# Optimization experiments

Hardware: AMD Instinct MI355X
Metric: run time of the kernel (lower is better)

The kernel has to match this reference:

```python
import jax, jax.numpy as jnp
import numpy as np

N, S, D, K = 4, 2048, 512, 16  # batch, seq_len, d_model, d_state


def setup_inputs() -> dict:
    key = jax.random.key(0)
    ks = jax.random.split(key, 6)
    tokens = jax.random.normal(ks[0], (N, S, D), dtype=jnp.float32)
    log_A = jax.random.normal(ks[1], (D, K), dtype=jnp.float32) * 0.1
    W_B = jax.random.normal(ks[2], (K, D), dtype=jnp.float32) * (1.0 / np.sqrt(D))
    W_C = jax.random.normal(ks[3], (K, D), dtype=jnp.float32) * (1.0 / np.sqrt(D))
    W_delta = jax.random.normal(ks[4], (D, D), dtype=jnp.float32) * (1.0 / np.sqrt(D))
    b_delta = jax.random.normal(ks[5], (D,), dtype=jnp.float32) * 0.01
    return {"tokens": tokens, "log_A": log_A, "W_B": W_B, "W_C": W_C,
            "W_delta": W_delta, "b_delta": b_delta}


def _selective_scan(toks, log_A, W_B, W_C, W_delta, b_delta):
    # toks: [N,S,D]
    deltas = jax.nn.softplus(toks @ W_delta.T + b_delta)          # [N,S,D]
    Bs = toks @ W_B.T                                             # [N,S,K]
    Cs = toks @ W_C.T                                             # [N,S,K]
    A_cont = -jnp.exp(log_A)                                      # [D,K]
    A_disc = jnp.exp(deltas[..., None] * A_cont)                  # [N,S,D,K]
    B_disc = deltas[..., None] * Bs[:, :, None, :]                # [N,S,D,K]

    def step(state, inp):
        a, b, x, c = inp  # a,b: [N,D,K]; x: [N,D]; c: [N,K]
        state = a * state + b * x[..., None]                      # [N,D,K]
        y = jnp.einsum('ndk,nk->nd', state, c)                    # [N,D]
        return state, y

    xs = (jnp.moveaxis(A_disc, 1, 0), jnp.moveaxis(B_disc, 1, 0),
          jnp.moveaxis(toks, 1, 0), jnp.moveaxis(Cs, 1, 0))
    init = jnp.zeros((toks.shape[0], log_A.shape[0], log_A.shape[1]), toks.dtype)
    _, ys = jax.lax.scan(step, init, xs)                          # ys: [S,N,D]
    return jnp.moveaxis(ys, 0, 1)                                 # [N,S,D]


def reference(tokens, log_A, W_B, W_C, W_delta, b_delta):
    out_fwd = _selective_scan(tokens, log_A, W_B, W_C, W_delta, b_delta)
    out_bwd = _selective_scan(jnp.flip(tokens, axis=1), log_A, W_B, W_C, W_delta, b_delta)
    out = out_fwd + jnp.flip(out_bwd, axis=1)                     # [N,S,D]
    return out.mean(axis=1)                                       # [N,D]
```

## Files before the change

kernel.cpp:

```cpp
#include <hip/hip_runtime.h>
#include <math.h>

#define NB   4
#define SEQ  2048
#define DM   512
#define KS   16
#define ROWS (NB*SEQ)

#define NCHUNK 16
#define CLEN   (SEQ / NCHUNK)
#define CH_TOT (2 * NB * NCHUNK * DM * KS)

typedef __attribute__((ext_vector_type(8))) short          bf16x8;
typedef __attribute__((ext_vector_type(8))) unsigned short u16x8;
typedef __attribute__((ext_vector_type(4))) float          f32x4;

__device__ __forceinline__ float softplus_f(float z) {
    return z > 20.f ? z : log1pf(__expf(z));
}

__device__ __forceinline__ unsigned short f2bf(float f) {
    unsigned int u = __builtin_bit_cast(unsigned int, f);
    u += 0x7fffu + ((u >> 16) & 1u);
    return (unsigned short)(u >> 16);
}

__global__ __launch_bounds__(256)
void k_cast_w(const float* __restrict__ src, unsigned short* __restrict__ dst, int n)
{
    const int i = (blockIdx.x * 256 + threadIdx.x) * 8;
    if (i >= n) return;
    const float4 a = *(const float4*)(src + i);
    const float4 b = *(const float4*)(src + i + 4);
    u16x8 v;
    v[0] = f2bf(a.x); v[1] = f2bf(a.y); v[2] = f2bf(a.z); v[3] = f2bf(a.w);
    v[4] = f2bf(b.x); v[5] = f2bf(b.y); v[6] = f2bf(b.z); v[7] = f2bf(b.w);
    *(u16x8*)(dst + i) = v;
}

#define GBM 128
#define GBN 128
#define GBK 32
#define PADK 40

__global__ __launch_bounds__(256)
void k_gemm_delta(const float* __restrict__ toks, const unsigned short* __restrict__ Wbf,
                  const float* __restrict__ bd,
                  float* __restrict__ odelta, float* __restrict__ odx)
{
    __shared__ unsigned short As[GBM][PADK];
    __shared__ unsigned short Bs[GBN][PADK];
    const int tid = threadIdx.x;
    const int rowBase = blockIdx.x * GBM;
    const int colBase = blockIdx.y * GBN;

    const int l   = tid & 63;
    const int wid = tid >> 6;
    const int wm  = wid >> 1;
    const int wn  = wid & 1;
    const int lr  = l & 15;
    const int lk  = (l >> 4) * 8;
    const int lq  = (l >> 4) * 4;

    const int srow  = tid >> 1;
    const int skoff = (tid & 1) * 16;

    const float*          gA = toks + (size_t)(rowBase + srow) * DM + skoff;
    const unsigned short* gW = Wbf  + (size_t)(colBase + srow) * DM + skoff;

    const f32x4 zero4 = {0.f, 0.f, 0.f, 0.f};
    f32x4 acc[4][4];
    #pragma unroll
    for (int i = 0; i < 4; ++i)
        #pragma unroll
        for (int j = 0; j < 4; ++j) acc[i][j] = zero4;

    float4 pa0 = *(const float4*)(gA);
    float4 pa1 = *(const float4*)(gA + 4);
    float4 pa2 = *(const float4*)(gA + 8);
    float4 pa3 = *(const float4*)(gA + 12);
    u16x8  pw0 = *(const u16x8*)(gW);
    u16x8  pw1 = *(const u16x8*)(gW + 8);

    for (int e0 = 0; e0 < DM; e0 += GBK) {
        __syncthreads();
        u16x8 va, vb;
        va[0] = f2bf(pa0.x); va[1] = f2bf(pa0.y); va[2] = f2bf(pa0.z); va[3] = f2bf(pa0.w);
        va[4] = f2bf(pa1.x); va[5] = f2bf(pa1.y); va[6] = f2bf(pa1.z); va[7] = f2bf(pa1.w);
        vb[0] = f2bf(pa2.x); vb[1] = f2bf(pa2.y); vb[2] = f2bf(pa2.z); vb[3] = f2bf(pa2.w);
        vb[4] = f2bf(pa3.x); vb[5] = f2bf(pa3.y); vb[6] = f2bf(pa3.z); vb[7] = f2bf(pa3.w);
        *(u16x8*)&As[srow][skoff]     = va;
        *(u16x8*)&As[srow][skoff + 8] = vb;
        *(u16x8*)&Bs[srow][skoff]     = pw0;
        *(u16x8*)&Bs[srow][skoff + 8] = pw1;
        __syncthreads();

        if (e0 + GBK < DM) {
            pa0 = *(const float4*)(gA + e0 + GBK);
            pa1 = *(const float4*)(gA + e0 + GBK + 4);
            pa2 = *(const float4*)(gA + e0 + GBK + 8);
            pa3 = *(const float4*)(gA + e0 + GBK + 12);
            pw0 = *(const u16x8*)(gW + e0 + GBK);
            pw1 = *(const u16x8*)(gW + e0 + GBK + 8);
        }

        bf16x8 af[4], bfr[4];
        #pragma unroll
        for (int f = 0; f < 4; ++f)
            af[f] = *(const bf16x8*)&As[wm * 64 + f * 16 + lr][lk];
        #pragma unroll
        for (int f = 0; f < 4; ++f)
            bfr[f] = *(const bf16x8*)&Bs[wn * 64 + f * 16 + lr][lk];

        #pragma unroll
        for (int fm = 0; fm < 4; ++fm)
            #pragma unroll
            for (int fn = 0; fn < 4; ++fn)
                acc[fm][fn] = __builtin_amdgcn_mfma_f32_16x16x32_bf16(
                    af[fm], bfr[fn], acc[fm][fn], 0, 0, 0);
    }

    #pragma unroll
    for (int fn = 0; fn < 4; ++fn) {
        const int col = colBase + wn * 64 + fn * 16 + lr;
        const float bias = bd[col];
        #pragma unroll
        for (int fm = 0; fm < 4; ++fm) {
            const int row0 = rowBase + wm * 64 + fm * 16 + lq;
            #pragma unroll
            for (int r = 0; r < 4; ++r) {
                const size_t off = (size_t)(row0 + r) * DM + col;
                const float dl = softplus_f(acc[fm][fn][r] + bias);
                odelta[off] = dl;
                odx[off]    = dl * toks[off];
            }
        }
    }
}

__global__ __launch_bounds__(256)
void k_bc(const float* __restrict__ toks, const float* __restrict__ WB,
          const float* __restrict__ WC, float* __restrict__ oB,
          float* __restrict__ oC)
{
    const int tid = threadIdx.x;
    const int k  = tid & 15;
    const int rl = tid >> 4;
    const int row = blockIdx.x * 16 + rl;
    const float* tp = toks + (size_t)row * DM;
    const float* wb = WB + (size_t)k * DM;
    const float* wc = WC + (size_t)k * DM;
    float ab = 0.f, ac = 0.f;
    #pragma unroll 4
    for (int e = 0; e < DM; e += 4) {
        float4 tv = *(const float4*)(tp + e);
        float4 bv = *(const float4*)(wb + e);
        float4 cv = *(const float4*)(wc + e);
        ab = fmaf(tv.x, bv.x, ab); ab = fmaf(tv.y, bv.y, ab);
        ab = fmaf(tv.z, bv.z, ab); ab = fmaf(tv.w, bv.w, ab);
        ac = fmaf(tv.x, cv.x, ac); ac = fmaf(tv.y, cv.y, ac);
        ac = fmaf(tv.z, cv.z, ac); ac = fmaf(tv.w, cv.w, ac);
    }
    oB[(size_t)row * KS + k] = ab;
    oC[(size_t)row * KS + k] = ac;
}

__global__ __launch_bounds__(256)
void k_scan_chunk(const float* __restrict__ de, const float* __restrict__ dx,
                  const float* __restrict__ Bsp, const float* __restrict__ Csp,
                  const float* __restrict__ logA,
                  float* __restrict__ oP, float* __restrict__ oQ,
                  float* __restrict__ oR, float* __restrict__ oS)
{
    const int g     = blockIdx.x * blockDim.x + threadIdx.x;
    const int k     = g & 15;
    const int d     = (g >> 4) & (DM - 1);
    const int chunk = (g >> 13) & (NCHUNK - 1);
    const int n     = (g >> 17) & (NB - 1);
    const int dir   = (g >> 19) & 1;

    const float Ac = -__expf(logA[d * KS + k]);

    const int sgn = dir ? -1 : 1;
    const int t0  = dir ? (SEQ - 1 - chunk * CLEN) : (chunk * CLEN);
    const size_t rbase = (size_t)n * SEQ + t0;

    const float* pd = de  + rbase * DM + d;
    const float* px = dx  + rbase * DM + d;
    const float* pb = Bsp + rbase * KS + k;
    const float* pc = Csp + rbase * KS + k;
    const int sD = sgn * DM;
    const int sK = sgn * KS;

    float A = 1.f, u = 0.f, R = 0.f, S = 0.f;
    #pragma unroll 4
    for (int t = 0; t < CLEN; ++t) {
        const float dev = *pd;
        const float bxv = *px;
        const float bv  = *pb;
        const float cv  = *pc;
        pd += sD; px += sD; pb += sK; pc += sK;
        const float a = __expf(dev * Ac);
        u = fmaf(a, u, bxv * bv);
        A = A * a;
        R = fmaf(cv, A, R);
        S = fmaf(cv, u, S);
    }

    const size_t idx = ((((size_t)dir * NB + n) * NCHUNK + chunk) * DM + d) * KS + k;
    oP[idx] = A; oQ[idx] = u; oR[idx] = R; oS[idx] = S;
}

__global__ __launch_bounds__(256)
void k_scan_fix(const float* __restrict__ oP, const float* __restrict__ oQ,
                const float* __restrict__ oR, const float* __restrict__ oS,
                float* __restrict__ out)
{
    const int g   = blockIdx.x * blockDim.x + threadIdx.x;
    const int k   = g & 15;
    const int d   = (g >> 4) & (DM - 1);
    const int n   = (g >> 13) & (NB - 1);
    const int dir = (g >> 15) & 1;

    size_t idx = ((((size_t)dir * NB + n) * NCHUNK) * DM + d) * KS + k;
    const size_t stride = (size_t)DM * KS;

    float h = 0.f, acc = 0.f;
    #pragma unroll
    for (int c = 0; c < NCHUNK; ++c) {
        const float P = oP[idx];
        const float Q = oQ[idx];
        const float R = oR[idx];
        const float S = oS[idx];
        idx += stride;
        acc = fmaf(R, h, acc) + S;
        h   = fmaf(P, h, Q);
    }

    acc += __shfl_xor(acc, 1);
    acc += __shfl_xor(acc, 2);
    acc += __shfl_xor(acc, 4);
    acc += __shfl_xor(acc, 8);

    if (k == 0)
        atomicAdd(&out[n * DM + d], acc * (1.0f / SEQ));
}

extern "C" void kernel_launch(void* const* d_in, const int* in_sizes, int n_in,
                              void* d_out, int out_size, void* d_ws, size_t ws_size,
                              hipStream_t stream) {
    const float* toks = (const float*)d_in[0];
    const float* logA = (const float*)d_in[1];
    const float* WB   = (const float*)d_in[2];
    const float* WC   = (const float*)d_in[3];
    const float* Wd   = (const float*)d_in[4];
    const float* bd   = (const float*)d_in[5];
    float* out = (float*)d_out;

    float* ws    = (float*)d_ws;
    float* wdel  = ws;
    float* wdx   = wdel + (size_t)ROWS * DM;
    float* wB    = wdx  + (size_t)ROWS * DM;
    float* wC    = wB   + (size_t)ROWS * KS;
    float* wP    = wC   + (size_t)ROWS * KS;
    float* wQ    = wP   + (size_t)CH_TOT;
    float* wR    = wQ   + (size_t)CH_TOT;
    float* wS    = wR   + (size_t)CH_TOT;
    unsigned short* wWbf = (unsigned short*)(wS + (size_t)CH_TOT);

    hipMemsetAsync(d_out, 0, sizeof(float) * NB * DM, stream);

    k_cast_w<<<(DM * DM) / (256 * 8), 256, 0, stream>>>(Wd, wWbf, DM * DM);
    k_gemm_delta<<<dim3(ROWS / GBM, DM / GBN), 256, 0, stream>>>(
        toks, wWbf, bd, wdel, wdx);
    k_bc<<<ROWS / 16, 256, 0, stream>>>(toks, WB, WC, wB, wC);
    k_scan_chunk<<<(2 * NB * NCHUNK * DM * KS) / 256, 256, 0, stream>>>(
        wdel, wdx, wB, wC, logA, wP, wQ, wR, wS);
    k_scan_fix<<<(2 * NB * DM * KS) / 256, 256, 0, stream>>>(wP, wQ, wR, wS, out);
}
```

Before: 248.9 us.

## Interleave delta/dx and B/C buffers, fuse weight cast, drop atomics

Stores delta and delta*x interleaved as float2, and B and C the same way, so each scan step issues two vector loads instead of four scalar streams. Drops the separate weight-cast kernel and converts W_delta to bf16 inside the GEMM tile load. Reorders the fix-up thread mapping so both directions for one (n,d) share a wavefront and sum by shuffle. The result is written directly, which removes the memset and the atomics. In exchange, every GEMM block re-reads the fp32 weights and converts them again, and the scan's strided loads now cover twice the bytes per row.

```diff
diff --git a/kernel.cpp b/kernel.cpp
--- a/kernel.cpp
+++ b/kernel.cpp
@@ -25,28 +25,14 @@
     return (unsigned short)(u >> 16);
 }
 
-__global__ __launch_bounds__(256)
-void k_cast_w(const float* __restrict__ src, unsigned short* __restrict__ dst, int n)
-{
-    const int i = (blockIdx.x * 256 + threadIdx.x) * 8;
-    if (i >= n) return;
-    const float4 a = *(const float4*)(src + i);
-    const float4 b = *(const float4*)(src + i + 4);
-    u16x8 v;
-    v[0] = f2bf(a.x); v[1] = f2bf(a.y); v[2] = f2bf(a.z); v[3] = f2bf(a.w);
-    v[4] = f2bf(b.x); v[5] = f2bf(b.y); v[6] = f2bf(b.z); v[7] = f2bf(b.w);
-    *(u16x8*)(dst + i) = v;
-}
-
 #define GBM 128
 #define GBN 128
 #define GBK 32
 #define PADK 40
 
 __global__ __launch_bounds__(256)
-void k_gemm_delta(const float* __restrict__ toks, const unsigned short* __restrict__ Wbf,
-                  const float* __restrict__ bd,
-                  float* __restrict__ odelta, float* __restrict__ odx)
+void k_gemm_delta(const float* __restrict__ toks, const float* __restrict__ Wd,
+                  const float* __restrict__ bd, float* __restrict__ odd)
 {
     __shared__ unsigned short As[GBM][PADK];
     __shared__ unsigned short Bs[GBN][PADK];
@@ -65,8 +51,8 @@
     const int srow  = tid >> 1;
     const int skoff = (tid & 1) * 16;
 
-    const float*          gA = toks + (size_t)(rowBase + srow) * DM + skoff;
-    const unsigned short* gW = Wbf  + (size_t)(colBase + srow) * DM + skoff;
+    const float* gA = toks + (size_t)(rowBase + srow) * DM + skoff;
+    const float* gW = Wd   + (size_t)(colBase + srow) * DM + skoff;
 
     const f32x4 zero4 = {0.f, 0.f, 0.f, 0.f};
     f32x4 acc[4][4];
@@ -79,20 +65,26 @@
     float4 pa1 = *(const float4*)(gA + 4);
     float4 pa2 = *(const float4*)(gA + 8);
     float4 pa3 = *(const float4*)(gA + 12);
-    u16x8  pw0 = *(const u16x8*)(gW);
-    u16x8  pw1 = *(const u16x8*)(gW + 8);
+    float4 pw0 = *(const float4*)(gW);
+    float4 pw1 = *(const float4*)(gW + 4);
+    float4 pw2 = *(const float4*)(gW + 8);
+    float4 pw3 = *(const float4*)(gW + 12);
 
     for (int e0 = 0; e0 < DM; e0 += GBK) {
         __syncthreads();
-        u16x8 va, vb;
+        u16x8 va, vb, vc, vd;
         va[0] = f2bf(pa0.x); va[1] = f2bf(pa0.y); va[2] = f2bf(pa0.z); va[3] = f2bf(pa0.w);
         va[4] = f2bf(pa1.x); va[5] = f2bf(pa1.y); va[6] = f2bf(pa1.z); va[7] = f2bf(pa1.w);
         vb[0] = f2bf(pa2.x); vb[1] = f2bf(pa2.y); vb[2] = f2bf(pa2.z); vb[3] = f2bf(pa2.w);
         vb[4] = f2bf(pa3.x); vb[5] = f2bf(pa3.y); vb[6] = f2bf(pa3.z); vb[7] = f2bf(pa3.w);
+        vc[0] = f2bf(pw0.x); vc[1] = f2bf(pw0.y); vc[2] = f2bf(pw0.z); vc[3] = f2bf(pw0.w);
+        vc[4] = f2bf(pw1.x); vc[5] = f2bf(pw1.y); vc[6] = f2bf(pw1.z); vc[7] = f2bf(pw1.w);
+        vd[0] = f2bf(pw2.x); vd[1] = f2bf(pw2.y); vd[2] = f2bf(pw2.z); vd[3] = f2bf(pw2.w);
+        vd[4] = f2bf(pw3.x); vd[5] = f2bf(pw3.y); vd[6] = f2bf(pw3.z); vd[7] = f2bf(pw3.w);
         *(u16x8*)&As[srow][skoff]     = va;
         *(u16x8*)&As[srow][skoff + 8] = vb;
-        *(u16x8*)&Bs[srow][skoff]     = pw0;
-        *(u16x8*)&Bs[srow][skoff + 8] = pw1;
+        *(u16x8*)&Bs[srow][skoff]     = vc;
+        *(u16x8*)&Bs[srow][skoff + 8] = vd;
         __syncthreads();
 
         if (e0 + GBK < DM) {
@@ -100,8 +92,10 @@
             pa1 = *(const float4*)(gA + e0 + GBK + 4);
             pa2 = *(const float4*)(gA + e0 + GBK + 8);
             pa3 = *(const float4*)(gA + e0 + GBK + 12);
-            pw0 = *(const u16x8*)(gW + e0 + GBK);
-            pw1 = *(const u16x8*)(gW + e0 + GBK + 8);
+            pw0 = *(const float4*)(gW + e0 + GBK);
+            pw1 = *(const float4*)(gW + e0 + GBK + 4);
+            pw2 = *(const float4*)(gW + e0 + GBK + 8);
+            pw3 = *(const float4*)(gW + e0 + GBK + 12);
         }
 
         bf16x8 af[4], bfr[4];
@@ -131,8 +125,7 @@
             for (int r = 0; r < 4; ++r) {
                 const size_t off = (size_t)(row0 + r) * DM + col;
                 const float dl = softplus_f(acc[fm][fn][r] + bias);
-                odelta[off] = dl;
-                odx[off]    = dl * toks[off];
+                *(float2*)&odd[2 * off] = make_float2(dl, dl * toks[off]);
             }
         }
     }
@@ -140,8 +133,7 @@
 
 __global__ __launch_bounds__(256)
 void k_bc(const float* __restrict__ toks, const float* __restrict__ WB,
-          const float* __restrict__ WC, float* __restrict__ oB,
-          float* __restrict__ oC)
+          const float* __restrict__ WC, float* __restrict__ obc)
 {
     const int tid = threadIdx.x;
     const int k  = tid & 15;
@@ -161,13 +153,11 @@
         ac = fmaf(tv.x, cv.x, ac); ac = fmaf(tv.y, cv.y, ac);
         ac = fmaf(tv.z, cv.z, ac); ac = fmaf(tv.w, cv.w, ac);
     }
-    oB[(size_t)row * KS + k] = ab;
-    oC[(size_t)row * KS + k] = ac;
-}
-
-__global__ __launch_bounds__(256)
-void k_scan_chunk(const float* __restrict__ de, const float* __restrict__ dx,
-                  const float* __restrict__ Bsp, const float* __restrict__ Csp,
+    *(float2*)&obc[2 * ((size_t)row * KS + k)] = make_float2(ab, ac);
+}
+
+__global__ __launch_bounds__(256)
+void k_scan_chunk(const float* __restrict__ dd, const float* __restrict__ bc,
                   const float* __restrict__ logA,
                   float* __restrict__ oP, float* __restrict__ oQ,
                   float* __restrict__ oR, float* __restrict__ oS)
@@ -185,26 +175,22 @@
     const int t0  = dir ? (SEQ - 1 - chunk * CLEN) : (chunk * CLEN);
     const size_t rbase = (size_t)n * SEQ + t0;
 
-    const float* pd = de  + rbase * DM + d;
-    const float* px = dx  + rbase * DM + d;
-    const float* pb = Bsp + rbase * KS + k;
-    const float* pc = Csp + rbase * KS + k;
-    const int sD = sgn * DM;
-    const int sK = sgn * KS;
+    const float* pd = dd + 2 * (rbase * DM + d);
+    const float* pb = bc + 2 * (rbase * KS + k);
+    const int sD = sgn * DM * 2;
+    const int sK = sgn * KS * 2;
 
     float A = 1.f, u = 0.f, R = 0.f, S = 0.f;
     #pragma unroll 4
     for (int t = 0; t < CLEN; ++t) {
-        const float dev = *pd;
-        const float bxv = *px;
-        const float bv  = *pb;
-        const float cv  = *pc;
-        pd += sD; px += sD; pb += sK; pc += sK;
-        const float a = __expf(dev * Ac);
-        u = fmaf(a, u, bxv * bv);
+        const float2 v = *(const float2*)pd;
+        const float2 w = *(const float2*)pb;
+        pd += sD; pb += sK;
+        const float a = __expf(v.x * Ac);
+        u = fmaf(a, u, v.y * w.x);
         A = A * a;
-        R = fmaf(cv, A, R);
-        S = fmaf(cv, u, S);
+        R = fmaf(w.y, A, R);
+        S = fmaf(w.y, u, S);
     }
 
     const size_t idx = ((((size_t)dir * NB + n) * NCHUNK + chunk) * DM + d) * KS + k;
@@ -216,11 +202,11 @@
                 const float* __restrict__ oR, const float* __restrict__ oS,
                 float* __restrict__ out)
 {
-    const int g   = blockIdx.x * blockDim.x + threadIdx.x;
-    const int k   = g & 15;
-    const int d   = (g >> 4) & (DM - 1);
-    const int n   = (g >> 13) & (NB - 1);
-    const int dir = (g >> 15) & 1;
+    const int g    = blockIdx.x * blockDim.x + threadIdx.x;
+    const int k    = g & 15;
+    const int dir  = (g >> 4) & 1;
+    const int d    = (g >> 5) & (DM - 1);
+    const int n    = (g >> 14) & (NB - 1);
 
     size_t idx = ((((size_t)dir * NB + n) * NCHUNK) * DM + d) * KS + k;
     const size_t stride = (size_t)DM * KS;
@@ -241,9 +227,10 @@
     acc += __shfl_xor(acc, 2);
     acc += __shfl_xor(acc, 4);
     acc += __shfl_xor(acc, 8);
-
-    if (k == 0)
-        atomicAdd(&out[n * DM + d], acc * (1.0f / SEQ));
+    acc += __shfl_xor(acc, 16);
+
+    if ((g & 31) == 0)
+        out[n * DM + d] = acc * (1.0f / SEQ);
 }
 
 extern "C" void kernel_launch(void* const* d_in, const int* in_sizes, int n_in,
@@ -257,24 +244,17 @@
     const float* bd   = (const float*)d_in[5];
     float* out = (float*)d_out;
 
-    float* ws    = (float*)d_ws;
-    float* wdel  = ws;
-    float* wdx   = wdel + (size_t)ROWS * DM;
-    float* wB    = wdx  + (size_t)ROWS * DM;
-    float* wC    = wB   + (size_t)ROWS * KS;
-    float* wP    = wC   + (size_t)ROWS * KS;
-    float* wQ    = wP   + (size_t)CH_TOT;
-    float* wR    = wQ   + (size_t)CH_TOT;
-    float* wS    = wR   + (size_t)CH_TOT;
-    unsigned short* wWbf = (unsigned short*)(wS + (size_t)CH_TOT);
-
-    hipMemsetAsync(d_out, 0, sizeof(float) * NB * DM, stream);
-
-    k_cast_w<<<(DM * DM) / (256 * 8), 256, 0, stream>>>(Wd, wWbf, DM * DM);
-    k_gemm_delta<<<dim3(ROWS / GBM, DM / GBN), 256, 0, stream>>>(
-        toks, wWbf, bd, wdel, wdx);
-    k_bc<<<ROWS / 16, 256, 0, stream>>>(toks, WB, WC, wB, wC);
+    float* ws   = (float*)d_ws;
+    float* wdd  = ws;
+    float* wbc  = wdd + (size_t)2 * ROWS * DM;
+    float* wP   = wbc + (size_t)2 * ROWS * KS;
+    float* wQ   = wP  + (size_t)CH_TOT;
+    float* wR   = wQ  + (size_t)CH_TOT;
+    float* wS   = wR  + (size_t)CH_TOT;
+
+    k_gemm_delta<<<dim3(ROWS / GBM, DM / GBN), 256, 0, stream>>>(toks, Wd, bd, wdd);
+    k_bc<<<ROWS / 16, 256, 0, stream>>>(toks, WB, WC, wbc);
     k_scan_chunk<<<(2 * NB * NCHUNK * DM * KS) / 256, 256, 0, stream>>>(
-        wdel, wdx, wB, wC, logA, wP, wQ, wR, wS);
-    k_scan_fix<<<(2 * NB * DM * KS) / 256, 256, 0, stream>>>(wP, wQ, wR, wS, out);
-}
+        wdd, wbc, logA, wP, wQ, wR, wS);
+    k_scan_fix<<<(NB * DM * 32) / 256, 256, 0, stream>>>(wP, wQ, wR, wS, out);
+}
```

After: 302.3 us. 21.5% more time.
